# Kernel tuning notes

Measured on AMD Instinct MI355X. Metric: run time of the kernel, lower is better.

## Reference

```python
import jax, jax.numpy as jnp
import numpy as np

# Model dims
B, T, D = 1, 2048, 2048          # batch, seq_len, d_model
HI, DI = 4, 64                   # indexer heads / dim
H, DH = 16, 128                  # attention heads / head dim (H*DH == D)
TOPK = 512                       # sparse top-k tokens per query
NEG = -1e9


def setup_inputs() -> dict:
    key = jax.random.key(0)
    ks = jax.random.split(key, 8)
    s = 0.02  # weight init scale
    return {
        "hidden_states": jax.random.normal(ks[0], (B, T, D), jnp.float32),
        "Wq_idx": jax.random.normal(ks[1], (D, HI * DI), jnp.float32) * s,
        "Wk_idx": jax.random.normal(ks[2], (D, DI), jnp.float32) * s,
        "Ww_idx": jax.random.normal(ks[3], (D, HI), jnp.float32) * s,
        "Wq": jax.random.normal(ks[4], (D, H * DH), jnp.float32) * s,
        "Wk": jax.random.normal(ks[5], (D, H * DH), jnp.float32) * s,
        "Wv": jax.random.normal(ks[6], (D, H * DH), jnp.float32) * s,
        "Wo": jax.random.normal(ks[7], (H * DH, D), jnp.float32) * s,
    }


def reference(hidden_states, Wq_idx, Wk_idx, Ww_idx, Wq, Wk, Wv, Wo):
    x = hidden_states
    # ---- Lightning indexer: I[t,s] = sum_j w[t,j] * relu(q[t,j] . k[s]) ----
    qi = (x @ Wq_idx).reshape(B, T, HI, DI)          # [B,T,HI,DI]
    ki = x @ Wk_idx                                   # [B,S,DI]
    w = x @ Ww_idx                                    # [B,T,HI]
    dots = jnp.einsum('bthd,bsd->bths', qi, ki)       # [B,T,HI,S]
    index_scores = (jax.nn.relu(dots) * w[..., None]).sum(axis=2)  # [B,T,S]

    # ---- Top-k token selection with causal mask ----
    causal = jnp.triu(jnp.ones((T, T), dtype=bool), 1)            # True above diag
    masked_scores = jnp.where(causal[None], NEG, index_scores)
    _, top_idx = jax.lax.top_k(masked_scores, TOPK)               # [B,T,TOPK]
    b_ix = jnp.arange(B)[:, None, None]
    t_ix = jnp.arange(T)[None, :, None]
    top_mask = jnp.zeros((B, T, T), dtype=bool).at[b_ix, t_ix, top_idx].set(True)
    add_mask = jnp.where(top_mask, 0.0, NEG).astype(x.dtype)      # [B,T,S]

    # ---- Dense multi-head attention with additive sparse mask ----
    q = (x @ Wq).reshape(B, T, H, DH)
    k = (x @ Wk).reshape(B, T, H, DH)
    v = (x @ Wv).reshape(B, T, H, DH)
    scores = jnp.einsum('bthd,bshd->bhts', q, k) / np.sqrt(DH).astype(np.float32)
    scores = scores + add_mask[:, None]                            # [B,H,T,S]
    probs = jax.nn.softmax(scores, axis=-1)
    attn = jnp.einsum('bhts,bshd->bthd', probs, v).reshape(B, T, H * DH)
    attn_output = attn @ Wo                                        # [B,T,D]
    return attn_output
```

## Files before the change

kernel.cpp:

```cpp
#include <hip/hip_runtime.h>
#include <cstdint>
#include <cstddef>

#define T_DIM 2048
#define D_DIM 2048
#define HI_N 4
#define DI_N 64
#define H_N 16
#define DH_N 128
#define TOPK_N 512
#define NEG_F (-1e9f)
#define FA_NEG (-1e30f)

typedef __attribute__((ext_vector_type(8))) short short8;
typedef __attribute__((ext_vector_type(4))) float f32x4;
typedef unsigned short ushort_t;

__device__ __forceinline__ unsigned short f2bf(float f) {
  unsigned u = __float_as_uint(f);
  u += 0x7FFFu + ((u >> 16) & 1u);
  return (unsigned short)(u >> 16);
}
__device__ __forceinline__ float bf2f(unsigned short b) {
  return __uint_as_float((unsigned)b << 16);
}

__global__ __launch_bounds__(256) void idx_proj(const float* __restrict__ x,
                                                const float* __restrict__ Wq_idx,
                                                const float* __restrict__ Wk_idx,
                                                const float* __restrict__ Ww_idx,
                                                float* __restrict__ qi,
                                                float* __restrict__ ki,
                                                float* __restrict__ wI) {
  __shared__ float As[2][16][64];
  __shared__ float Bs[2][16][64];
  const int bm = blockIdx.y << 6;
  const int bn_id = blockIdx.x;
  const float* B; float* C; int ldB, cb, ncols;
  if (bn_id < 4)       { B = Wq_idx; C = qi; ldB = 256; cb = bn_id << 6; ncols = 64; }
  else if (bn_id == 4) { B = Wk_idx; C = ki; ldB = 64;  cb = 0;          ncols = 64; }
  else                 { B = Ww_idx; C = wI; ldB = 4;   cb = 0;          ncols = 4;  }
  const int tid = threadIdx.x;
  const int tx = tid & 15, ty = tid >> 4;
  const int am = tid >> 2;
  const int ak = (tid & 3) << 2;
  float acc[4][4] = {};

  float4 a4 = *(const float4*)&x[(size_t)(bm + am) * 2048 + ak];
  float4 b4 = make_float4(0, 0, 0, 0);
  if ((tx << 2) < ncols) b4 = *(const float4*)&B[(size_t)ty * ldB + cb + (tx << 2)];
  As[0][ak + 0][am] = a4.x; As[0][ak + 1][am] = a4.y;
  As[0][ak + 2][am] = a4.z; As[0][ak + 3][am] = a4.w;
  *(float4*)&Bs[0][ty][tx << 2] = b4;

  int p = 0;
  for (int k0 = 0; k0 < 2048; k0 += 16) {
    __syncthreads();
    const bool more = (k0 + 16) < 2048;
    if (more) {
      a4 = *(const float4*)&x[(size_t)(bm + am) * 2048 + k0 + 16 + ak];
      if ((tx << 2) < ncols)
        b4 = *(const float4*)&B[(size_t)(k0 + 16 + ty) * ldB + cb + (tx << 2)];
    }
#pragma unroll
    for (int kk = 0; kk < 16; ++kk) {
      float4 av4 = *(const float4*)&As[p][kk][ty << 2];
      float4 bv4 = *(const float4*)&Bs[p][kk][tx << 2];
      float av[4] = {av4.x, av4.y, av4.z, av4.w};
      float bv[4] = {bv4.x, bv4.y, bv4.z, bv4.w};
#pragma unroll
      for (int i = 0; i < 4; ++i)
#pragma unroll
        for (int j = 0; j < 4; ++j) acc[i][j] += av[i] * bv[j];
    }
    if (more) {
      As[1 - p][ak + 0][am] = a4.x; As[1 - p][ak + 1][am] = a4.y;
      As[1 - p][ak + 2][am] = a4.z; As[1 - p][ak + 3][am] = a4.w;
      *(float4*)&Bs[1 - p][ty][tx << 2] = b4;
    }
    p ^= 1;
  }
#pragma unroll
  for (int i = 0; i < 4; ++i) {
    int m = bm + (ty << 2) + i;
    int n0 = tx << 2;
    if (n0 + 3 < ncols) {
      *(float4*)&C[(size_t)m * ldB + cb + n0] =
          make_float4(acc[i][0], acc[i][1], acc[i][2], acc[i][3]);
    } else {
#pragma unroll
      for (int j = 0; j < 4; ++j)
        if (n0 + j < ncols) C[(size_t)m * ldB + cb + n0 + j] = acc[i][j];
    }
  }
}

__global__ __launch_bounds__(256) void cast_bf16(const float* __restrict__ in,
                                                 ushort_t* __restrict__ out) {
  int i = (blockIdx.x * 256 + threadIdx.x) * 4;
  float4 f = *(const float4*)(in + i);
  ushort4 o;
  o.x = f2bf(f.x); o.y = f2bf(f.y); o.z = f2bf(f.z); o.w = f2bf(f.w);
  *(ushort4*)(out + i) = o;
}

__global__ __launch_bounds__(256) void cast_transpose(const float* __restrict__ in,
                                                      ushort_t* __restrict__ out,
                                                      int R, int C) {
  __shared__ float tile[32][33];
  const int bx = blockIdx.x * 32;
  const int by = blockIdx.y * 32;
  const int tx = threadIdx.x & 31, ty = threadIdx.x >> 5;
#pragma unroll
  for (int i = 0; i < 32; i += 8)
    tile[ty + i][tx] = in[(size_t)(by + ty + i) * C + bx + tx];
  __syncthreads();
#pragma unroll
  for (int i = 0; i < 32; i += 8)
    out[(size_t)(bx + ty + i) * R + by + tx] = f2bf(tile[tx][ty + i]);
}

__global__ __launch_bounds__(256) void transpose_bf(const ushort_t* __restrict__ in,
                                                    ushort_t* __restrict__ out,
                                                    int ldin) {
  __shared__ ushort_t tile[64][68];
  const int bx = blockIdx.x * 64;
  const int by = blockIdx.y * 64;
  const int tid = threadIdx.x;
#pragma unroll
  for (int p = 0; p < 4; ++p) {
    int r = p * 16 + (tid >> 4), c0 = (tid & 15) * 4;
    *(ushort4*)&tile[r][c0] = *(const ushort4*)(in + (size_t)(by + r) * ldin + bx + c0);
  }
  __syncthreads();
#pragma unroll
  for (int p = 0; p < 4; ++p) {
    int r = p * 16 + (tid >> 4), c0 = (tid & 15) * 4;
    ushort4 o;
    o.x = tile[c0 + 0][r]; o.y = tile[c0 + 1][r];
    o.z = tile[c0 + 2][r]; o.w = tile[c0 + 3][r];
    *(ushort4*)(out + (size_t)(bx + r) * T_DIM + by + c0) = o;
  }
}

template <int OUT_BF16>
__global__ __launch_bounds__(256) void gemm_bt(const ushort_t* __restrict__ A,
                                               const ushort_t* __restrict__ Bt,
                                               void* __restrict__ C,
                                               int M, int N, int K) {
  __shared__ __attribute__((aligned(16))) ushort_t As[128 * 64];
  __shared__ __attribute__((aligned(16))) ushort_t Bs[128 * 64];
  const int bm = blockIdx.y << 7;
  const int bn = blockIdx.x << 7;
  const int tid = threadIdx.x;
  const int lane = tid & 63;
  const int wv = tid >> 6;
  const int wm = (wv >> 1) << 6;
  const int wn = (wv & 1) << 6;

  f32x4 acc[4][4] = {};

  const int sr = tid >> 3;
  const int sc = (tid & 7) << 3;
  const ushort_t* ga = A + (size_t)(bm + sr) * K + sc;
  const ushort_t* gb = Bt + (size_t)(bn + sr) * K + sc;
  const size_t rstep = (size_t)32 * K;

  for (int k0 = 0; k0 < K; k0 += 64) {
#pragma unroll
    for (int i = 0; i < 4; ++i) {
      __builtin_amdgcn_global_load_lds(
          (const __attribute__((address_space(1))) unsigned int*)(ga + i * rstep + k0),
          (__attribute__((address_space(3))) unsigned int*)(As + i * 2048 + tid * 8),
          16, 0, 0);
      __builtin_amdgcn_global_load_lds(
          (const __attribute__((address_space(1))) unsigned int*)(gb + i * rstep + k0),
          (__attribute__((address_space(3))) unsigned int*)(Bs + i * 2048 + tid * 8),
          16, 0, 0);
    }
    __syncthreads();
#pragma unroll
    for (int ks = 0; ks < 2; ++ks) {
      short8 af[4], bfr[4];
      const int kk = (ks << 5) + ((lane >> 4) << 3);
#pragma unroll
      for (int i = 0; i < 4; ++i) {
        af[i]  = *(const short8*)(As + (wm + (i << 4) + (lane & 15)) * 64 + kk);
        bfr[i] = *(const short8*)(Bs + (wn + (i << 4) + (lane & 15)) * 64 + kk);
      }
#pragma unroll
      for (int i = 0; i < 4; ++i)
#pragma unroll
        for (int j = 0; j < 4; ++j)
          acc[i][j] = __builtin_amdgcn_mfma_f32_16x16x32_bf16(af[i], bfr[j], acc[i][j], 0, 0, 0);
    }
    __syncthreads();
  }

  const int lrow = (lane >> 4) << 2;
  const int lcol = lane & 15;
#pragma unroll
  for (int i = 0; i < 4; ++i) {
    const int row = bm + wm + (i << 4) + lrow;
#pragma unroll
    for (int j = 0; j < 4; ++j) {
      const int col = bn + wn + (j << 4) + lcol;
#pragma unroll
      for (int r = 0; r < 4; ++r) {
        if (OUT_BF16)
          ((ushort_t*)C)[(size_t)(row + r) * N + col] = f2bf(acc[i][j][r]);
        else
          ((float*)C)[(size_t)(row + r) * N + col] = acc[i][j][r];
      }
    }
  }
}

__global__ __launch_bounds__(256) void idx_scores_rt(const float* __restrict__ qi,
                                                     const float* __restrict__ ki,
                                                     const float* __restrict__ w,
                                                     float* __restrict__ out) {
  const int t0 = blockIdx.y << 6, s0 = blockIdx.x << 6;
  const int tid = threadIdx.x;
  const int tx = tid & 15, ty = tid >> 4;
  if (s0 > t0 + 63) {
    const float4 nf = make_float4(NEG_F, NEG_F, NEG_F, NEG_F);
#pragma unroll
    for (int i = 0; i < 4; ++i) {
      int m = t0 + (ty << 2) + i;
      *(float4*)&out[(size_t)m * T_DIM + s0 + (tx << 2)] = nf;
    }
    return;
  }
  __shared__ float As[16][64];
  __shared__ float Bs[16][64];
  __shared__ float wsh[64][4];
  if (tid < 64) *(float4*)wsh[tid] = *(const float4*)&w[(size_t)(t0 + tid) * 4];
  const int am = tid >> 2;
  const int ak = (tid & 3) << 2;
  float oacc[4][4] = {};
#pragma unroll
  for (int h = 0; h < HI_N; ++h) {
    float dacc[4][4] = {};
    for (int k0 = 0; k0 < DI_N; k0 += 16) {
      float4 qa = *(const float4*)&qi[(size_t)(t0 + am) * 256 + h * DI_N + k0 + ak];
      float4 kb = *(const float4*)&ki[(size_t)(s0 + am) * DI_N + k0 + ak];
      __syncthreads();
      As[ak + 0][am] = qa.x; As[ak + 1][am] = qa.y;
      As[ak + 2][am] = qa.z; As[ak + 3][am] = qa.w;
      Bs[ak + 0][am] = kb.x; Bs[ak + 1][am] = kb.y;
      Bs[ak + 2][am] = kb.z; Bs[ak + 3][am] = kb.w;
      __syncthreads();
#pragma unroll
      for (int kk = 0; kk < 16; ++kk) {
        float4 a4 = *(const float4*)&As[kk][ty << 2];
        float4 b4 = *(const float4*)&Bs[kk][tx << 2];
        float av[4] = {a4.x, a4.y, a4.z, a4.w};
        float bv[4] = {b4.x, b4.y, b4.z, b4.w};
#pragma unroll
        for (int i = 0; i < 4; ++i)
#pragma unroll
          for (int j = 0; j < 4; ++j) dacc[i][j] += av[i] * bv[j];
      }
    }
#pragma unroll
    for (int i = 0; i < 4; ++i) {
      float wh = wsh[(ty << 2) + i][h];
#pragma unroll
      for (int j = 0; j < 4; ++j) oacc[i][j] += fmaxf(dacc[i][j], 0.f) * wh;
    }
  }
#pragma unroll
  for (int i = 0; i < 4; ++i) {
    int m = t0 + (ty << 2) + i;
    int n0 = s0 + (tx << 2);
    float4 r;
    r.x = (n0 + 0 > m) ? NEG_F : oacc[i][0];
    r.y = (n0 + 1 > m) ? NEG_F : oacc[i][1];
    r.z = (n0 + 2 > m) ? NEG_F : oacc[i][2];
    r.w = (n0 + 3 > m) ? NEG_F : oacc[i][3];
    *(float4*)&out[(size_t)m * T_DIM + n0] = r;
  }
}

__global__ __launch_bounds__(256) void select_mask(const float* __restrict__ scores,
                                                   unsigned long long* __restrict__ maskbits) {
  const int t = blockIdx.x, tid = threadIdx.x;
  __shared__ unsigned int hist[256];
  __shared__ unsigned int s_prefix, s_krem;
  __shared__ unsigned char bytes[256];
  unsigned int uv[8];
  const float* row = scores + (size_t)t * T_DIM;
  {
    float4 f0 = *(const float4*)(row + tid * 8);
    float4 f1 = *(const float4*)(row + tid * 8 + 4);
    float fv[8] = {f0.x, f0.y, f0.z, f0.w, f1.x, f1.y, f1.z, f1.w};
#pragma unroll
    for (int j = 0; j < 8; ++j) {
      unsigned u = __float_as_uint(fv[j]);
      uv[j] = (u & 0x80000000u) ? ~u : (u | 0x80000000u);
    }
  }
  if (tid == 0) { s_prefix = 0u; s_krem = TOPK_N; }
  for (int p = 0; p < 4; ++p) {
    const int sh = 24 - 8 * p;
    hist[tid] = 0;
    __syncthreads();
    const unsigned pm = p ? (0xFFFFFFFFu << (32 - 8 * p)) : 0u;
    const unsigned prefix = s_prefix;
#pragma unroll
    for (int j = 0; j < 8; ++j)
      if ((uv[j] & pm) == prefix) atomicAdd(&hist[(uv[j] >> sh) & 255], 1u);
    __syncthreads();
    if (tid == 0) {
      unsigned krem = s_krem, cum = 0;
      int b = 255;
      for (;; --b) { cum += hist[b]; if (cum >= krem) break; }
      s_prefix = prefix | ((unsigned)b << sh);
      s_krem = krem - (cum - hist[b]);
    }
    __syncthreads();
  }
  const unsigned V = s_prefix;
  const int kr = (int)s_krem;
  int eqc = 0;
#pragma unroll
  for (int j = 0; j < 8; ++j) eqc += (uv[j] == V);
  __syncthreads();
  hist[tid] = (unsigned)eqc;
  __syncthreads();
  for (int off = 1; off < 256; off <<= 1) {
    int v = (int)hist[tid];
    if (tid >= off) v += (int)hist[tid - off];
    __syncthreads();
    hist[tid] = (unsigned)v;
    __syncthreads();
  }
  int run = (int)hist[tid] - eqc;
  unsigned char byte = 0;
#pragma unroll
  for (int j = 0; j < 8; ++j) {
    bool eq = (uv[j] == V);
    bool take = (uv[j] > V) || (eq && run < kr);
    run += eq;
    byte |= (unsigned char)(take ? (1u << j) : 0u);
  }
  bytes[tid] = byte;
  __syncthreads();
  if (tid < 32) {
    unsigned long long wqw = 0;
#pragma unroll
    for (int b = 0; b < 8; ++b)
      wqw |= (unsigned long long)bytes[tid * 8 + b] << (8 * b);
    maskbits[(size_t)t * 32 + tid] = wqw;
  }
}

__global__ __launch_bounds__(256, 1) void flash_attn(
    const ushort_t* __restrict__ q, const ushort_t* __restrict__ k,
    const ushort_t* __restrict__ vt, const unsigned long long* __restrict__ maskbits,
    ushort_t* __restrict__ attn, int ldqk) {
  __shared__ __attribute__((aligned(16))) ushort_t Ks[2][128 * 128];
  __shared__ __attribute__((aligned(16))) ushort_t Vts[128 * 128];
  __shared__ __attribute__((aligned(16))) ushort_t Ps[128 * 136];

  const int tt = blockIdx.x;
  const int h  = blockIdx.y;
  const int t0 = tt << 7;
  const int tid = threadIdx.x;
  const int lane = tid & 63;
  const int wv = tid >> 6;
  const int l15 = lane & 15, l4 = lane >> 4;
  const int e3 = l15 & 7;
  const int scol = (((tid & 15) ^ ((tid >> 4) & 7)) << 3);

  {
    const ushort_t* gq = q + (size_t)(t0 + (tid >> 4)) * ldqk + h * DH_N + scol;
#pragma unroll
    for (int p = 0; p < 8; ++p)
      __builtin_amdgcn_global_load_lds(
          (const __attribute__((address_space(1))) unsigned int*)(gq + (size_t)p * 16 * ldqk),
          (__attribute__((address_space(3))) unsigned int*)(Ks[0] + p * 2048 + tid * 8), 16, 0, 0);
  }
  asm volatile("s_waitcnt vmcnt(0)" ::: "memory");
  __builtin_amdgcn_s_barrier();
  asm volatile("" ::: "memory");
  short8 qfrag[4][2];
#pragma unroll
  for (int ks = 0; ks < 4; ++ks)
#pragma unroll
    for (int j = 0; j < 2; ++j)
      qfrag[ks][j] = *(const short8*)(Ks[0] + (wv * 32 + j * 16 + l15) * 128 +
                                      ((((ks << 2) + l4) ^ e3) << 3));
  asm volatile("s_waitcnt lgkmcnt(0)" ::: "memory");
  __builtin_amdgcn_s_barrier();
  asm volatile("" ::: "memory");

  f32x4 acc[8][2] = {};
  float m_reg[2] = {-INFINITY, -INFINITY};
  float l_reg[2] = {0.f, 0.f};
  const int nst = (tt < 4) ? 4 : (tt + 1);
  const float rsc = 0.08838834764831845f;

  {
    const ushort_t* gk = k + (size_t)(tid >> 4) * ldqk + h * DH_N + scol;
#pragma unroll
    for (int p = 0; p < 8; ++p)
      __builtin_amdgcn_global_load_lds(
          (const __attribute__((address_space(1))) unsigned int*)(gk + (size_t)p * 16 * ldqk),
          (__attribute__((address_space(3))) unsigned int*)(Ks[0] + p * 2048 + tid * 8), 16, 0, 0);
  }

  for (int st = 0; st < nst; ++st) {
    const int s0 = st << 7;
    const bool pf = (st + 1) < nst;

    asm volatile("" ::: "memory");
    __builtin_amdgcn_s_barrier();
    asm volatile("" ::: "memory");

    unsigned long long mw[2][2];
    {
      const int wbase = s0 >> 6;
#pragma unroll
      for (int j = 0; j < 2; ++j)
#pragma unroll
        for (int wd = 0; wd < 2; ++wd)
          mw[j][wd] = maskbits[(size_t)(t0 + wv * 32 + j * 16 + l15) * 32 + wbase + wd];
    }
    {
      const ushort_t* gv = vt + (size_t)(h * DH_N + (tid >> 4)) * T_DIM + s0 + scol;
#pragma unroll
      for (int p = 0; p < 8; ++p)
        __builtin_amdgcn_global_load_lds(
            (const __attribute__((address_space(1))) unsigned int*)(gv + (size_t)p * 16 * T_DIM),
            (__attribute__((address_space(3))) unsigned int*)(Vts + p * 2048 + tid * 8), 16, 0, 0);
    }
    asm volatile("" ::: "memory");
    if (pf) {
      const ushort_t* gk = k + (size_t)(s0 + 128 + (tid >> 4)) * ldqk + h * DH_N + scol;
      ushort_t* dst = Ks[(st + 1) & 1];
#pragma unroll
      for (int p = 0; p < 8; ++p)
        __builtin_amdgcn_global_load_lds(
            (const __attribute__((address_space(1))) unsigned int*)(gk + (size_t)p * 16 * ldqk),
            (__attribute__((address_space(3))) unsigned int*)(dst + p * 2048 + tid * 8), 16, 0, 0);
    }
    if (pf) asm volatile("s_waitcnt vmcnt(20)" ::: "memory");
    else    asm volatile("s_waitcnt vmcnt(12)" ::: "memory");
    __builtin_amdgcn_s_barrier();
    asm volatile("" ::: "memory");

    const ushort_t* Kb = Ks[st & 1];
    f32x4 sacc[8][2] = {};
    __builtin_amdgcn_s_setprio(1);
#pragma unroll
    for (int ks = 0; ks < 4; ++ks) {
      const int co = ((((ks << 2) + l4) ^ e3) << 3);
      short8 af[8];
#pragma unroll
      for (int i = 0; i < 8; ++i)
        af[i] = *(const short8*)(Kb + (i * 16 + l15) * 128 + co);
#pragma unroll
      for (int i = 0; i < 8; ++i)
#pragma unroll
        for (int j = 0; j < 2; ++j)
          sacc[i][j] = __builtin_amdgcn_mfma_f32_16x16x32_bf16(af[i], qfrag[ks][j], sacc[i][j], 0, 0, 0);
    }
    __builtin_amdgcn_s_setprio(0);

#pragma unroll
    for (int i = 0; i < 8; ++i)
#pragma unroll
      for (int j = 0; j < 2; ++j)
#pragma unroll
        for (int r = 0; r < 4; ++r) {
          bool sel = (mw[j][i >> 2] >> ((i & 3) * 16 + l4 * 4 + r)) & 1;
          sacc[i][j][r] = sel ? sacc[i][j][r] * rsc : FA_NEG;
        }

    float alpha[2];
#pragma unroll
    for (int j = 0; j < 2; ++j) {
      float pm = sacc[0][j][0];
#pragma unroll
      for (int i = 0; i < 8; ++i)
#pragma unroll
        for (int r = 0; r < 4; ++r) pm = fmaxf(pm, sacc[i][j][r]);
      pm = fmaxf(pm, __shfl_xor(pm, 16));
      pm = fmaxf(pm, __shfl_xor(pm, 32));
      const float mn = fmaxf(m_reg[j], pm);
      alpha[j] = __expf(m_reg[j] - mn);
      float ps = 0.f;
#pragma unroll
      for (int i = 0; i < 8; ++i)
#pragma unroll
        for (int r = 0; r < 4; ++r) {
          float s = sacc[i][j][r];
          float pv = (s <= -1e29f) ? 0.f : __expf(s - mn);
          sacc[i][j][r] = pv;
          ps += pv;
        }
      ps += __shfl_xor(ps, 16);
      ps += __shfl_xor(ps, 32);
      l_reg[j] = alpha[j] * l_reg[j] + ps;
      m_reg[j] = mn;
    }
#pragma unroll
    for (int i = 0; i < 8; ++i)
#pragma unroll
      for (int j = 0; j < 2; ++j)
#pragma unroll
        for (int r = 0; r < 4; ++r) acc[i][j][r] *= alpha[j];

#pragma unroll
    for (int j = 0; j < 2; ++j)
#pragma unroll
      for (int i = 0; i < 8; ++i) {
        ushort4 pk;
        pk.x = f2bf(sacc[i][j][0]); pk.y = f2bf(sacc[i][j][1]);
        pk.z = f2bf(sacc[i][j][2]); pk.w = f2bf(sacc[i][j][3]);
        *(ushort4*)&Ps[(wv * 32 + j * 16 + l15) * 136 + i * 16 + l4 * 4] = pk;
      }

    if (pf) asm volatile("s_waitcnt vmcnt(8)" ::: "memory");
    else    asm volatile("s_waitcnt vmcnt(0)" ::: "memory");
    __builtin_amdgcn_s_barrier();
    asm volatile("" ::: "memory");

    __builtin_amdgcn_s_setprio(1);
#pragma unroll
    for (int ks = 0; ks < 4; ++ks) {
      const int co = ((((ks << 2) + l4) ^ e3) << 3);
      short8 af[8], bq[2];
#pragma unroll
      for (int i = 0; i < 8; ++i)
        af[i] = *(const short8*)(Vts + (i * 16 + l15) * 128 + co);
#pragma unroll
      for (int j = 0; j < 2; ++j)
        bq[j] = *(const short8*)(Ps + (wv * 32 + j * 16 + l15) * 136 + ks * 32 + l4 * 8);
#pragma unroll
      for (int i = 0; i < 8; ++i)
#pragma unroll
        for (int j = 0; j < 2; ++j)
          acc[i][j] = __builtin_amdgcn_mfma_f32_16x16x32_bf16(af[i], bq[j], acc[i][j], 0, 0, 0);
    }
    __builtin_amdgcn_s_setprio(0);
  }

  float linv[2];
#pragma unroll
  for (int j = 0; j < 2; ++j) linv[j] = 1.f / l_reg[j];
#pragma unroll
  for (int j = 0; j < 2; ++j)
#pragma unroll
    for (int i = 0; i < 8; ++i) {
      ushort4 pk;
      pk.x = f2bf(acc[i][j][0] * linv[j]);
      pk.y = f2bf(acc[i][j][1] * linv[j]);
      pk.z = f2bf(acc[i][j][2] * linv[j]);
      pk.w = f2bf(acc[i][j][3] * linv[j]);
      *(ushort4*)&Ps[(wv * 32 + j * 16 + l15) * 136 + i * 16 + l4 * 4] = pk;
    }
  __syncthreads();
#pragma unroll
  for (int p = 0; p < 8; ++p) {
    int rw = p * 16 + (tid >> 4);
    int d0 = (tid & 15) * 8;
    *(ulonglong2*)(attn + (size_t)(t0 + rw) * D_DIM + h * DH_N + d0) =
        *(const ulonglong2*)(Ps + rw * 136 + d0);
  }
}

extern "C" void kernel_launch(void* const* d_in, const int* in_sizes, int n_in,
                              void* d_out, int out_size, void* d_ws, size_t ws_size,
                              hipStream_t stream) {
  (void)in_sizes; (void)n_in; (void)out_size; (void)ws_size;
  const float* x      = (const float*)d_in[0];
  const float* Wq_idx = (const float*)d_in[1];
  const float* Wk_idx = (const float*)d_in[2];
  const float* Ww_idx = (const float*)d_in[3];
  const float* Wq     = (const float*)d_in[4];
  const float* Wk     = (const float*)d_in[5];
  const float* Wv     = (const float*)d_in[6];
  const float* Wo     = (const float*)d_in[7];
  float* out = (float*)d_out;

  char* ws = (char*)d_ws;
  const size_t MB = 1ull << 20;
  float*    scores  = (float*)(ws);
  ushort_t* qkv_bf  = (ushort_t*)(ws);
  unsigned long long* maskbits = (unsigned long long*)(ws + 25 * MB + 512 * 1024);
  ushort_t* x_bf    = (ushort_t*)(ws + 26 * MB);
  ushort_t* Wcat_t  = (ushort_t*)(ws + 34 * MB);
  ushort_t* vt_bf   = (ushort_t*)(ws + 34 * MB);
  ushort_t* attn_bf = (ushort_t*)(ws + 42 * MB);
  ushort_t* Wo_t    = (ushort_t*)(ws + 58 * MB);
  float*    qi      = (float*)(ws + 66 * MB);
  float*    ki      = (float*)(ws + 68 * MB);
  float*    wI      = (float*)(ws + 68 * MB + 512 * 1024);

  const dim3 blk(256);
  const dim3 tgrid(D_DIM / 32, D_DIM / 32);

  cast_bf16<<<dim3((D_DIM * T_DIM) / 1024), blk, 0, stream>>>(x, x_bf);
  cast_transpose<<<tgrid, blk, 0, stream>>>(Wq, Wcat_t, D_DIM, D_DIM);
  cast_transpose<<<tgrid, blk, 0, stream>>>(Wk, Wcat_t + (size_t)D_DIM * D_DIM, D_DIM, D_DIM);
  cast_transpose<<<tgrid, blk, 0, stream>>>(Wv, Wcat_t + (size_t)2 * D_DIM * D_DIM, D_DIM, D_DIM);
  cast_transpose<<<tgrid, blk, 0, stream>>>(Wo, Wo_t, D_DIM, D_DIM);

  idx_proj<<<dim3(6, T_DIM / 64), blk, 0, stream>>>(x, Wq_idx, Wk_idx, Ww_idx, qi, ki, wI);
  idx_scores_rt<<<dim3(T_DIM / 64, T_DIM / 64), blk, 0, stream>>>(qi, ki, wI, scores);
  select_mask<<<dim3(T_DIM), blk, 0, stream>>>(scores, maskbits);

  gemm_bt<1><<<dim3(3 * D_DIM / 128, T_DIM / 128), blk, 0, stream>>>(
      x_bf, Wcat_t, qkv_bf, T_DIM, 3 * D_DIM, D_DIM);

  transpose_bf<<<dim3(D_DIM / 64, T_DIM / 64), blk, 0, stream>>>(
      qkv_bf + 2 * D_DIM, vt_bf, 3 * D_DIM);

  flash_attn<<<dim3(T_DIM / 128, H_N), blk, 0, stream>>>(
      qkv_bf, qkv_bf + D_DIM, vt_bf, maskbits, attn_bf, 3 * D_DIM);

  gemm_bt<0><<<dim3(D_DIM / 128, T_DIM / 128), blk, 0, stream>>>(
      attn_bf, Wo_t, out, T_DIM, D_DIM, D_DIM);
}
```

Baseline: 545.3 us.

## Replace QKV projection GEMM with 256x256-tile, 8-wave pipelined bf16 MFMA kernel

Adds a new GEMM kernel for the fused QKV projection. It uses 256x256 output tiles with 512 threads, double-buffered LDS with an XOR swizzle, and a fine-grained phase schedule. Global-to-LDS loads for the next k-tile are interleaved with the MFMA phases, controlled by explicit vmcnt waits and barriers. The aim is more data reuse per loaded byte, fewer LDS bank conflicts and better overlap of memory with compute than the 128x128 single-buffered gemm_bt. The trade-off is a grid of only 192 blocks, heavy register pressure and a hand-tuned wait schedule that is fragile.

After: 527.6 us. 3.2% less time.

```diff
diff --git a/kernel.cpp b/kernel.cpp
--- a/kernel.cpp
+++ b/kernel.cpp
@@ -24,6 +24,10 @@
 __device__ __forceinline__ float bf2f(unsigned short b) {
   return __uint_as_float((unsigned)b << 16);
 }
+
+#define GLDS(g, l) __builtin_amdgcn_global_load_lds( \
+    (const __attribute__((address_space(1))) unsigned int*)(g), \
+    (__attribute__((address_space(3))) unsigned int*)(l), 16, 0, 0)
 
 __global__ __launch_bounds__(256) void idx_proj(const float* __restrict__ x,
                                                 const float* __restrict__ Wq_idx,
@@ -169,14 +173,8 @@
   for (int k0 = 0; k0 < K; k0 += 64) {
 #pragma unroll
     for (int i = 0; i < 4; ++i) {
-      __builtin_amdgcn_global_load_lds(
-          (const __attribute__((address_space(1))) unsigned int*)(ga + i * rstep + k0),
-          (__attribute__((address_space(3))) unsigned int*)(As + i * 2048 + tid * 8),
-          16, 0, 0);
-      __builtin_amdgcn_global_load_lds(
-          (const __attribute__((address_space(1))) unsigned int*)(gb + i * rstep + k0),
-          (__attribute__((address_space(3))) unsigned int*)(Bs + i * 2048 + tid * 8),
-          16, 0, 0);
+      GLDS(ga + i * rstep + k0, As + i * 2048 + tid * 8);
+      GLDS(gb + i * rstep + k0, Bs + i * 2048 + tid * 8);
     }
     __syncthreads();
 #pragma unroll
@@ -212,6 +210,112 @@
         else
           ((float*)C)[(size_t)(row + r) * N + col] = acc[i][j][r];
       }
+    }
+  }
+}
+
+__global__ __launch_bounds__(512, 2) void gemm256_bt(const ushort_t* __restrict__ A,
+                                                     const ushort_t* __restrict__ Bt,
+                                                     ushort_t* __restrict__ C,
+                                                     int M, int N, int K) {
+  __shared__ __attribute__((aligned(16))) ushort_t Ab[2][256 * 64];
+  __shared__ __attribute__((aligned(16))) ushort_t Bb[2][256 * 64];
+  const int bm = blockIdx.y << 8;
+  const int bn = blockIdx.x << 8;
+  const int tid = threadIdx.x;
+  const int lane = tid & 63;
+  const int wid = tid >> 6;
+  const int wr = wid >> 2;
+  const int wc = wid & 3;
+  const int l15 = lane & 15, l4 = lane >> 4;
+  const int srow = tid >> 3;
+  const int schunk = tid & 7;
+  const int swc = (schunk ^ (srow & 7)) << 3;
+  const int NT = K >> 6;
+
+  f32x4 acc[8][4] = {};
+
+#define STAGE_A(b, h, kt) { \
+    const ushort_t* g_ = A + (size_t)(bm + (h) * 64 + srow) * K + (kt) * 64 + swc; \
+    GLDS(g_, Ab[b] + ((h) * 64 + srow) * 64 + (schunk << 3)); \
+    GLDS(g_ + (size_t)128 * K, Ab[b] + (128 + (h) * 64 + srow) * 64 + (schunk << 3)); }
+
+#define STAGE_B(b, h, kt) { \
+    const int br_ = ((srow >= 32) ? 64 : 0) + (h) * 32 + (srow & 31); \
+    const ushort_t* g_ = Bt + (size_t)(bn + br_) * K + (kt) * 64 + swc; \
+    GLDS(g_, Bb[b] + br_ * 64 + (schunk << 3)); \
+    GLDS(g_ + (size_t)128 * K, Bb[b] + (128 + br_) * 64 + (schunk << 3)); }
+
+#define VMW(n) asm volatile("s_waitcnt vmcnt(" #n ")" ::: "memory")
+
+#define PHASE(b, qm, qn, STG, WT) { \
+    short8 paf[4][2], pbf[2][2]; \
+    _Pragma("unroll") for (int m_ = 0; m_ < 4; ++m_) { \
+      const int Ra_ = wr * 128 + (qm) * 64 + m_ * 16 + l15; \
+      _Pragma("unroll") for (int ks_ = 0; ks_ < 2; ++ks_) \
+        paf[m_][ks_] = *(const short8*)(Ab[b] + Ra_ * 64 + ((((ks_ << 2) + l4) ^ (Ra_ & 7)) << 3)); } \
+    _Pragma("unroll") for (int n_ = 0; n_ < 2; ++n_) { \
+      const int Rb_ = wc * 64 + (qn) * 32 + n_ * 16 + l15; \
+      _Pragma("unroll") for (int ks_ = 0; ks_ < 2; ++ks_) \
+        pbf[n_][ks_] = *(const short8*)(Bb[b] + Rb_ * 64 + ((((ks_ << 2) + l4) ^ (Rb_ & 7)) << 3)); } \
+    STG; \
+    WT; \
+    asm volatile("" ::: "memory"); \
+    __builtin_amdgcn_s_barrier(); \
+    asm volatile("s_waitcnt lgkmcnt(0)" ::: "memory"); \
+    __builtin_amdgcn_sched_barrier(0); \
+    __builtin_amdgcn_s_setprio(1); \
+    _Pragma("unroll") for (int m_ = 0; m_ < 4; ++m_) \
+      _Pragma("unroll") for (int n_ = 0; n_ < 2; ++n_) \
+        _Pragma("unroll") for (int ks_ = 0; ks_ < 2; ++ks_) \
+          acc[(qm) * 4 + m_][(qn) * 2 + n_] = __builtin_amdgcn_mfma_f32_16x16x32_bf16( \
+              paf[m_][ks_], pbf[n_][ks_], acc[(qm) * 4 + m_][(qn) * 2 + n_], 0, 0, 0); \
+    __builtin_amdgcn_s_setprio(0); \
+    asm volatile("" ::: "memory"); \
+    __builtin_amdgcn_s_barrier(); \
+    asm volatile("" ::: "memory"); }
+
+  STAGE_A(0, 0, 0); STAGE_B(0, 0, 0); STAGE_A(0, 1, 0); STAGE_B(0, 1, 0);
+  STAGE_A(1, 0, 1); STAGE_B(1, 0, 1);
+  VMW(8);
+  asm volatile("" ::: "memory");
+  __builtin_amdgcn_s_barrier();
+  asm volatile("" ::: "memory");
+
+  for (int j = 0; j < NT / 2 - 1; ++j) {
+    const int t = j * 2;
+    PHASE(0, 0, 0, STAGE_A(1, 1, t + 1), VMW(6));
+    PHASE(0, 0, 1, STAGE_B(1, 1, t + 1), );
+    PHASE(0, 1, 0, STAGE_A(0, 0, t + 2), );
+    PHASE(0, 1, 1, STAGE_B(0, 0, t + 2), VMW(8));
+    PHASE(1, 0, 0, STAGE_A(0, 1, t + 2), VMW(6));
+    PHASE(1, 0, 1, STAGE_B(0, 1, t + 2), );
+    PHASE(1, 1, 0, STAGE_A(1, 0, t + 3), );
+    PHASE(1, 1, 1, STAGE_B(1, 0, t + 3), VMW(8));
+  }
+  PHASE(0, 0, 0, STAGE_A(1, 1, NT - 1), VMW(6));
+  PHASE(0, 0, 1, STAGE_B(1, 1, NT - 1), );
+  PHASE(0, 1, 0, , );
+  PHASE(0, 1, 1, , VMW(4));
+  PHASE(1, 0, 0, , VMW(0));
+  PHASE(1, 0, 1, , );
+  PHASE(1, 1, 0, , );
+  PHASE(1, 1, 1, , );
+
+#undef STAGE_A
+#undef STAGE_B
+#undef VMW
+#undef PHASE
+
+#pragma unroll
+  for (int i = 0; i < 8; ++i) {
+    const int row = bm + wr * 128 + i * 16 + l4 * 4;
+#pragma unroll
+    for (int j2 = 0; j2 < 4; ++j2) {
+      const int col = bn + wc * 64 + j2 * 16 + l15;
+#pragma unroll
+      for (int r = 0; r < 4; ++r)
+        C[(size_t)(row + r) * N + col] = f2bf(acc[i][j2][r]);
     }
   }
 }
@@ -378,9 +482,7 @@
     const ushort_t* gq = q + (size_t)(t0 + (tid >> 4)) * ldqk + h * DH_N + scol;
 #pragma unroll
     for (int p = 0; p < 8; ++p)
-      __builtin_amdgcn_global_load_lds(
-          (const __attribute__((address_space(1))) unsigned int*)(gq + (size_t)p * 16 * ldqk),
-          (__attribute__((address_space(3))) unsigned int*)(Ks[0] + p * 2048 + tid * 8), 16, 0, 0);
+      GLDS(gq + (size_t)p * 16 * ldqk, Ks[0] + p * 2048 + tid * 8);
   }
   asm volatile("s_waitcnt vmcnt(0)" ::: "memory");
   __builtin_amdgcn_s_barrier();
@@ -406,9 +508,7 @@
     const ushort_t* gk = k + (size_t)(tid >> 4) * ldqk + h * DH_N + scol;
 #pragma unroll
     for (int p = 0; p < 8; ++p)
-      __builtin_amdgcn_global_load_lds(
-          (const __attribute__((address_space(1))) unsigned int*)(gk + (size_t)p * 16 * ldqk),
-          (__attribute__((address_space(3))) unsigned int*)(Ks[0] + p * 2048 + tid * 8), 16, 0, 0);
+      GLDS(gk + (size_t)p * 16 * ldqk, Ks[0] + p * 2048 + tid * 8);
   }
 
   for (int st = 0; st < nst; ++st) {
@@ -432,9 +532,7 @@
       const ushort_t* gv = vt + (size_t)(h * DH_N + (tid >> 4)) * T_DIM + s0 + scol;
 #pragma unroll
       for (int p = 0; p < 8; ++p)
-        __builtin_amdgcn_global_load_lds(
-            (const __attribute__((address_space(1))) unsigned int*)(gv + (size_t)p * 16 * T_DIM),
-            (__attribute__((address_space(3))) unsigned int*)(Vts + p * 2048 + tid * 8), 16, 0, 0);
+        GLDS(gv + (size_t)p * 16 * T_DIM, Vts + p * 2048 + tid * 8);
     }
     asm volatile("" ::: "memory");
     if (pf) {
@@ -442,9 +540,7 @@
       ushort_t* dst = Ks[(st + 1) & 1];
 #pragma unroll
       for (int p = 0; p < 8; ++p)
-        __builtin_amdgcn_global_load_lds(
-            (const __attribute__((address_space(1))) unsigned int*)(gk + (size_t)p * 16 * ldqk),
-            (__attribute__((address_space(3))) unsigned int*)(dst + p * 2048 + tid * 8), 16, 0, 0);
+        GLDS(gk + (size_t)p * 16 * ldqk, dst + p * 2048 + tid * 8);
     }
     if (pf) asm volatile("s_waitcnt vmcnt(20)" ::: "memory");
     else    asm volatile("s_waitcnt vmcnt(12)" ::: "memory");
@@ -613,7 +709,7 @@
   idx_scores_rt<<<dim3(T_DIM / 64, T_DIM / 64), blk, 0, stream>>>(qi, ki, wI, scores);
   select_mask<<<dim3(T_DIM), blk, 0, stream>>>(scores, maskbits);
 
-  gemm_bt<1><<<dim3(3 * D_DIM / 128, T_DIM / 128), blk, 0, stream>>>(
+  gemm256_bt<<<dim3(3 * D_DIM / 256, T_DIM / 256), dim3(512), 0, stream>>>(
       x_bf, Wcat_t, qkv_bf, T_DIM, 3 * D_DIM, D_DIM);
 
   transpose_bf<<<dim3(D_DIM / 64, T_DIM / 64), blk, 0, stream>>>(
```
